# Optimization experiments

Measured on AMD Instinct MI355X. Metric: run time of the kernel, lower is better.

Reference implementation:

```python
import jax, jax.numpy as jnp
import numpy as np

N_NODES = 100000


def gcn_conv(x, src, dst, W, b, n_nodes):
    """PyG GCNConv: add self-loops, symmetric deg^-1/2 normalization,
    linear transform, scatter-add aggregation, bias."""
    loop = jnp.arange(n_nodes, dtype=src.dtype)
    s = jnp.concatenate([src, loop])
    d = jnp.concatenate([dst, loop])
    # degree of destination nodes (includes self-loops)
    deg = jax.ops.segment_sum(jnp.ones(s.shape[0], dtype=x.dtype), d,
                              num_segments=n_nodes)
    dis = jnp.where(deg > 0, jax.lax.rsqrt(deg), 0.0)  # deg^-1/2
    norm = dis[s] * dis[d]                              # [E+N]
    h = x @ W                                           # [N, out]
    msg = h[s] * norm[:, None]                          # gather + scale
    out = jax.ops.segment_sum(msg, d, num_segments=n_nodes)  # scatter-add
    return out + b


def setup_inputs() -> dict:
    key = jax.random.key(0)
    k1, k2, k3, k4 = jax.random.split(key, 4)
    F_in, H, C = 500, 64, 10
    x = jax.random.normal(k1, (N_NODES, F_in), dtype=jnp.float32)
    edge_index = jax.random.randint(k2, (2, 1600000), 0, N_NODES,
                                    dtype=jnp.int32)
    W1 = jax.random.normal(k3, (F_in, H), dtype=jnp.float32) / np.sqrt(F_in)
    b1 = jnp.zeros((H,), dtype=jnp.float32)
    W2 = jax.random.normal(k4, (H, C), dtype=jnp.float32) / np.sqrt(H)
    b2 = jnp.zeros((C,), dtype=jnp.float32)
    return {"x": x, "edge_index": edge_index,
            "W1": W1, "b1": b1, "W2": W2, "b2": b2}


def reference(x, edge_index, W1, b1, W2, b2):
    src, dst = edge_index[0], edge_index[1]
    h = gcn_conv(x, src, dst, W1, b1, N_NODES)
    h = jax.nn.relu(h)
    # dropout is identity at inference (training=False)
    out = gcn_conv(h, src, dst, W2, b2, N_NODES)
    return out
```

## Files before the change

### kernel.cpp

```cpp
#include <hip/hip_runtime.h>

#define F_IN 500
#define HDIM 64
#define CDIM 10
#define KPAD 512
#define NSTAGE 16

typedef __attribute__((ext_vector_type(8))) short bf16x8;
typedef __attribute__((ext_vector_type(4))) float floatx4;

__device__ inline unsigned short f2bf(float f) {
    unsigned int u = __float_as_uint(f);
    u += 0x7fffu + ((u >> 16) & 1u);
    return (unsigned short)(u >> 16);
}

__global__ void deg_count_kernel(const int* __restrict__ dst, int E,
                                 int* __restrict__ deg) {
    int e = blockIdx.x * blockDim.x + threadIdx.x;
    if (e < E) atomicAdd(&deg[dst[e]], 1);
}

__global__ void scan_block_kernel(const int* __restrict__ deg,
                                  int* __restrict__ row_ptr,
                                  int* __restrict__ blk_sum,
                                  float* __restrict__ dis, int Np1) {
    __shared__ int wsum[16];
    int i = blockIdx.x * 1024 + threadIdx.x;
    int v = (i < Np1 - 1) ? deg[i] : 0;
    if (i < Np1 - 1) dis[i] = rsqrtf((float)(v + 1));
    int lane = threadIdx.x & 63;
    int wid = threadIdx.x >> 6;
    int x = v;
#pragma unroll
    for (int off = 1; off < 64; off <<= 1) {
        int y = __shfl_up(x, off);
        if (lane >= off) x += y;
    }
    if (lane == 63) wsum[wid] = x;
    __syncthreads();
    if (threadIdx.x < 16) {
        int ws = wsum[threadIdx.x];
#pragma unroll
        for (int off = 1; off < 16; off <<= 1) {
            int y = __shfl_up(ws, off);
            if ((int)threadIdx.x >= off) ws += y;
        }
        wsum[threadIdx.x] = ws;
    }
    __syncthreads();
    int wp = (wid > 0) ? wsum[wid - 1] : 0;
    if (i < Np1) row_ptr[i] = wp + x - v;
    if (threadIdx.x == 1023) blk_sum[blockIdx.x] = wp + x;
}

__global__ void scan_top_kernel(int* __restrict__ blk_sum, int nb) {
    int carry = 0;
    for (int base = 0; base < nb; base += 64) {
        int i = base + (int)threadIdx.x;
        int v = (i < nb) ? blk_sum[i] : 0;
        int x = v;
#pragma unroll
        for (int off = 1; off < 64; off <<= 1) {
            int y = __shfl_up(x, off);
            if ((int)threadIdx.x >= off) x += y;
        }
        if (i < nb) blk_sum[i] = carry + x - v;
        carry += __shfl(x, 63);
    }
}

__global__ void scan_add_kernel(int* __restrict__ row_ptr,
                                const int* __restrict__ blk_sum, int Np1) {
    int i = blockIdx.x * blockDim.x + threadIdx.x;
    if (i < Np1) row_ptr[i] += blk_sum[i >> 10];
}

__global__ void csr_fill_kernel(const int* __restrict__ src,
                                const int* __restrict__ dst,
                                const int* __restrict__ row_ptr,
                                int* __restrict__ cursor,
                                int* __restrict__ csr_src, int E) {
    int e = blockIdx.x * blockDim.x + threadIdx.x;
    if (e >= E) return;
    int d = dst[e];
    int pos = atomicAdd(&cursor[d], 1);
    csr_src[row_ptr[d] + pos] = src[e];
}

__global__ void wprep_kernel(const float* __restrict__ W1,
                             unsigned short* __restrict__ whf,
                             unsigned short* __restrict__ wlf) {
    int idx = blockIdx.x * 256 + threadIdx.x;
    if (idx >= KPAD * HDIM) return;
    int k = idx >> 6;
    int f = idx & 63;
    float w = (k < F_IN) ? W1[k * HDIM + f] : 0.f;
    unsigned int b = __float_as_uint(w);
    unsigned short hh = (unsigned short)(b >> 16);
    float wl = w - __uint_as_float(b & 0xffff0000u);
    unsigned short ll = (unsigned short)(__float_as_uint(wl) >> 16);
    int kb = k >> 5, q = (k >> 3) & 3, j = k & 7;
    int fb = f >> 4, fl = f & 15;
    int lane = (q << 4) | fl;
    size_t o = ((((size_t)kb * 4 + fb) * 64 + lane) << 3) | (size_t)j;
    whf[o] = hh;
    wlf[o] = ll;
}

__global__ __launch_bounds__(256) void gemm1_kernel(
        const float* __restrict__ x,
        const unsigned short* __restrict__ whf,
        const unsigned short* __restrict__ wlf,
        const float* __restrict__ dis,
        unsigned short* __restrict__ h1b, int N) {
    const int lane = threadIdx.x & 63;
    const int wid = (blockIdx.x * 256 + threadIdx.x) >> 6;
    const int n0 = wid * 32;
    if (n0 >= N) return;
    const int q = lane >> 4;
    const int fl = lane & 15;

    int r0 = n0 + fl;       if (r0 >= N) r0 = N - 1;
    int r1 = n0 + 16 + fl;  if (r1 >= N) r1 = N - 1;
    const float* xp0 = x + (size_t)r0 * F_IN + q * 8;
    const float* xp1 = x + (size_t)r1 * F_IN + q * 8;

    floatx4 acc[2][4];
#pragma unroll
    for (int t = 0; t < 2; ++t)
#pragma unroll
        for (int fb = 0; fb < 4; ++fb) acc[t][fb] = (floatx4){0.f, 0.f, 0.f, 0.f};

    const bf16x8* whv = (const bf16x8*)whf;
    const bf16x8* wlv = (const bf16x8*)wlf;

    for (int kb = 0; kb < NSTAGE; ++kb) {
        float xv0[8], xv1[8];
        if (kb < NSTAGE - 1) {
            float4 a = *(const float4*)(xp0 + kb * 32);
            float4 b = *(const float4*)(xp0 + kb * 32 + 4);
            xv0[0] = a.x; xv0[1] = a.y; xv0[2] = a.z; xv0[3] = a.w;
            xv0[4] = b.x; xv0[5] = b.y; xv0[6] = b.z; xv0[7] = b.w;
            float4 c = *(const float4*)(xp1 + kb * 32);
            float4 d = *(const float4*)(xp1 + kb * 32 + 4);
            xv1[0] = c.x; xv1[1] = c.y; xv1[2] = c.z; xv1[3] = c.w;
            xv1[4] = d.x; xv1[5] = d.y; xv1[6] = d.z; xv1[7] = d.w;
        } else {
#pragma unroll
            for (int j = 0; j < 8; ++j) {
                int kk = kb * 32 + q * 8 + j;
                xv0[j] = (kk < F_IN) ? xp0[kb * 32 + j] : 0.f;
                xv1[j] = (kk < F_IN) ? xp1[kb * 32 + j] : 0.f;
            }
        }
        bf16x8 xh0, xl0, xh1, xl1;
#pragma unroll
        for (int j = 0; j < 8; ++j) {
            unsigned int b0 = __float_as_uint(xv0[j]);
            xh0[j] = (short)(b0 >> 16);
            float res0 = xv0[j] - __uint_as_float(b0 & 0xffff0000u);
            xl0[j] = (short)(__float_as_uint(res0) >> 16);
            unsigned int b1 = __float_as_uint(xv1[j]);
            xh1[j] = (short)(b1 >> 16);
            float res1 = xv1[j] - __uint_as_float(b1 & 0xffff0000u);
            xl1[j] = (short)(__float_as_uint(res1) >> 16);
        }
#pragma unroll
        for (int fb = 0; fb < 4; ++fb) {
            bf16x8 bh = whv[(size_t)(kb * 4 + fb) * 64 + lane];
            bf16x8 bl = wlv[(size_t)(kb * 4 + fb) * 64 + lane];
            acc[0][fb] = __builtin_amdgcn_mfma_f32_16x16x32_bf16(xh0, bh, acc[0][fb], 0, 0, 0);
            acc[0][fb] = __builtin_amdgcn_mfma_f32_16x16x32_bf16(xl0, bh, acc[0][fb], 0, 0, 0);
            acc[0][fb] = __builtin_amdgcn_mfma_f32_16x16x32_bf16(xh0, bl, acc[0][fb], 0, 0, 0);
            acc[1][fb] = __builtin_amdgcn_mfma_f32_16x16x32_bf16(xh1, bh, acc[1][fb], 0, 0, 0);
            acc[1][fb] = __builtin_amdgcn_mfma_f32_16x16x32_bf16(xl1, bh, acc[1][fb], 0, 0, 0);
            acc[1][fb] = __builtin_amdgcn_mfma_f32_16x16x32_bf16(xh1, bl, acc[1][fb], 0, 0, 0);
        }
    }
#pragma unroll
    for (int t = 0; t < 2; ++t) {
#pragma unroll
        for (int r = 0; r < 4; ++r) {
            int node = n0 + t * 16 + q * 4 + r;
            if (node < N) {
                float dn = dis[node];
#pragma unroll
                for (int fb = 0; fb < 4; ++fb) {
                    h1b[(size_t)node * HDIM + fb * 16 + fl] =
                        f2bf(acc[t][fb][r] * dn);
                }
            }
        }
    }
}

__global__ void gather1_kernel(const int* __restrict__ row_ptr,
                               const int* __restrict__ csr_src,
                               const float* __restrict__ dis,
                               const unsigned short* __restrict__ h1b,
                               float* __restrict__ agg1, int N) {
    int nid = blockIdx.x * 4 + (threadIdx.x >> 6);
    if (nid >= N) return;
    int node = __builtin_amdgcn_readfirstlane(nid);
    int lane = threadIdx.x & 63;
    int half = lane >> 5;
    int c = lane & 31;
    int beg = row_ptr[node];
    int end = row_ptr[node + 1];
    float dd = dis[node];
    float a0 = 0.f, a1 = 0.f;
    if (half == 0) {
        unsigned int w = *reinterpret_cast<const unsigned int*>(
            h1b + (size_t)node * HDIM + 2 * c);
        a0 = __uint_as_float(w << 16);
        a1 = __uint_as_float(w & 0xffff0000u);
    }
    int p = beg + half;
    for (; p + 6 < end; p += 8) {
        int s0 = csr_src[p];
        int s1 = csr_src[p + 2];
        int s2 = csr_src[p + 4];
        int s3 = csr_src[p + 6];
        unsigned int w0 = *reinterpret_cast<const unsigned int*>(h1b + (size_t)s0 * HDIM + 2 * c);
        unsigned int w1 = *reinterpret_cast<const unsigned int*>(h1b + (size_t)s1 * HDIM + 2 * c);
        unsigned int w2 = *reinterpret_cast<const unsigned int*>(h1b + (size_t)s2 * HDIM + 2 * c);
        unsigned int w3 = *reinterpret_cast<const unsigned int*>(h1b + (size_t)s3 * HDIM + 2 * c);
        a0 += __uint_as_float(w0 << 16);
        a1 += __uint_as_float(w0 & 0xffff0000u);
        a0 += __uint_as_float(w1 << 16);
        a1 += __uint_as_float(w1 & 0xffff0000u);
        a0 += __uint_as_float(w2 << 16);
        a1 += __uint_as_float(w2 & 0xffff0000u);
        a0 += __uint_as_float(w3 << 16);
        a1 += __uint_as_float(w3 & 0xffff0000u);
    }
    for (; p < end; p += 2) {
        int s0 = csr_src[p];
        unsigned int w0 = *reinterpret_cast<const unsigned int*>(h1b + (size_t)s0 * HDIM + 2 * c);
        a0 += __uint_as_float(w0 << 16);
        a1 += __uint_as_float(w0 & 0xffff0000u);
    }
    a0 += __shfl_xor(a0, 32);
    a1 += __shfl_xor(a1, 32);
    if (half == 0) {
        *reinterpret_cast<float2*>(agg1 + (size_t)node * HDIM + 2 * c) =
            make_float2(a0 * dd, a1 * dd);
    }
}

__global__ void layer2_kernel(const float* __restrict__ agg1,
                              const float* __restrict__ b1,
                              const float* __restrict__ W2,
                              const float* __restrict__ dis,
                              float* __restrict__ h2s, int N) {
    int n = blockIdx.x * blockDim.x + threadIdx.x;
    if (n >= N) return;
    const float* ar = agg1 + (size_t)n * HDIM;
    float t[HDIM];
#pragma unroll
    for (int c = 0; c < HDIM; ++c) {
        float v = ar[c] + b1[c];
        t[c] = v > 0.f ? v : 0.f;
    }
    float dn = dis[n];
    float* h2r = h2s + (size_t)n * CDIM;
#pragma unroll
    for (int j = 0; j < CDIM; ++j) {
        float acc = 0.f;
#pragma unroll
        for (int c = 0; c < HDIM; ++c) acc = fmaf(t[c], W2[c * CDIM + j], acc);
        h2r[j] = acc * dn;
    }
}

__global__ void gather2_kernel(const int* __restrict__ row_ptr,
                               const int* __restrict__ csr_src,
                               const float* __restrict__ dis,
                               const float* __restrict__ h2s,
                               const float* __restrict__ b2,
                               float* __restrict__ out, int N) {
    int nid = blockIdx.x * 4 + (threadIdx.x >> 6);
    if (nid >= N) return;
    int node = __builtin_amdgcn_readfirstlane(nid);
    int lane = threadIdx.x & 63;
    int g = lane >> 4;
    int j = lane & 15;
    int jj = (j < CDIM) ? j : CDIM - 1;
    int beg = row_ptr[node];
    int end = row_ptr[node + 1];
    float acc = 0.f;
    for (int p = beg + g; p < end; p += 4) {
        int s = csr_src[p];
        acc += h2s[(size_t)s * CDIM + jj];
    }
    acc += __shfl_xor(acc, 16);
    acc += __shfl_xor(acc, 32);
    if (lane < CDIM) {
        float dd = dis[node];
        out[(size_t)node * CDIM + lane] =
            b2[lane] + dd * (acc + h2s[(size_t)node * CDIM + lane]);
    }
}

static inline char* align256(char* p) {
    return (char*)(((uintptr_t)p + 255) & ~(uintptr_t)255);
}

extern "C" void kernel_launch(void* const* d_in, const int* in_sizes, int n_in,
                              void* d_out, int out_size, void* d_ws,
                              size_t ws_size, hipStream_t stream) {
    const float* x  = (const float*)d_in[0];
    const int*   ei = (const int*)d_in[1];
    const float* W1 = (const float*)d_in[2];
    const float* b1 = (const float*)d_in[3];
    const float* W2 = (const float*)d_in[4];
    const float* b2 = (const float*)d_in[5];

    const int N = in_sizes[0] / F_IN;
    const int E = in_sizes[1] / 2;
    const int* src = ei;
    const int* dst = ei + E;
    float* out = (float*)d_out;

    const int Np1 = N + 1;
    const int nscan_blocks = (Np1 + 1023) / 1024;

    char* w = (char*)d_ws;
    int* deg = (int*)w;                  w = align256(w + (size_t)N * 4);
    int* cursor = (int*)w;               w = align256(w + (size_t)N * 4);
    float* dis = (float*)w;              w = align256(w + (size_t)N * 4);
    int* row_ptr = (int*)w;              w = align256(w + (size_t)(N + 4) * 4);
    int* blk_sum = (int*)w;              w = align256(w + (size_t)nscan_blocks * 4);
    int* csr_src = (int*)w;              w = align256(w + (size_t)E * 4);
    unsigned short* whf = (unsigned short*)w;  w = align256(w + (size_t)KPAD * HDIM * 2);
    unsigned short* wlf = (unsigned short*)w;  w = align256(w + (size_t)KPAD * HDIM * 2);
    unsigned short* h1b = (unsigned short*)w;  w = align256(w + (size_t)N * HDIM * 2);
    float* agg1 = (float*)w;             w = align256(w + (size_t)N * HDIM * 4);
    float* h2s = (float*)h1b;

    hipMemsetAsync(deg, 0, (size_t)N * 2 * 4, stream);
    hipMemsetAsync(cursor, 0, (size_t)N * 4, stream);

    wprep_kernel<<<(KPAD * HDIM + 255) / 256, 256, 0, stream>>>(W1, whf, wlf);
    deg_count_kernel<<<(E + 255) / 256, 256, 0, stream>>>(dst, E, deg);
    scan_block_kernel<<<nscan_blocks, 1024, 0, stream>>>(deg, row_ptr, blk_sum,
                                                         dis, Np1);
    scan_top_kernel<<<1, 64, 0, stream>>>(blk_sum, nscan_blocks);
    scan_add_kernel<<<(Np1 + 255) / 256, 256, 0, stream>>>(row_ptr, blk_sum,
                                                           Np1);
    csr_fill_kernel<<<(E + 255) / 256, 256, 0, stream>>>(src, dst, row_ptr,
                                                         cursor, csr_src, E);
    {
        int nwaves = (N + 31) / 32;
        int blocks = (nwaves + 3) / 4;
        gemm1_kernel<<<blocks, 256, 0, stream>>>(x, whf, wlf, dis, h1b, N);
    }
    gather1_kernel<<<(N + 3) / 4, 256, 0, stream>>>(row_ptr, csr_src, dis, h1b,
                                                    agg1, N);
    layer2_kernel<<<(N + 255) / 256, 256, 0, stream>>>(agg1, b1, W2, dis, h2s,
                                                       N);
    gather2_kernel<<<(N + 3) / 4, 256, 0, stream>>>(row_ptr, csr_src, dis, h2s,
                                                    b2, out, N);
}
```

Before: 587.4 us.

## Merge prep, CSR fill and GEMM launches; pad h2 rows; deepen gather unrolling

```diff
diff --git a/kernel.cpp b/kernel.cpp
--- a/kernel.cpp
+++ b/kernel.cpp
@@ -5,6 +5,7 @@
 #define CDIM 10
 #define KPAD 512
 #define NSTAGE 16
+#define H2LD 16
 
 typedef __attribute__((ext_vector_type(8))) short bf16x8;
 typedef __attribute__((ext_vector_type(4))) float floatx4;
@@ -14,11 +15,34 @@
     u += 0x7fffu + ((u >> 16) & 1u);
     return (unsigned short)(u >> 16);
 }
-
-__global__ void deg_count_kernel(const int* __restrict__ dst, int E,
-                                 int* __restrict__ deg) {
-    int e = blockIdx.x * blockDim.x + threadIdx.x;
-    if (e < E) atomicAdd(&deg[dst[e]], 1);
+__device__ inline float bflo(unsigned int u) { return __uint_as_float(u << 16); }
+__device__ inline float bfhi(unsigned int u) { return __uint_as_float(u & 0xffff0000u); }
+
+__global__ __launch_bounds__(256) void prep_kernel(
+        const int* __restrict__ dst, int E, int* __restrict__ deg,
+        const float* __restrict__ W1, unsigned short* __restrict__ whf,
+        unsigned short* __restrict__ wlf, int degB) {
+    int bid = blockIdx.x;
+    if (bid < degB) {
+        int e = bid * 256 + threadIdx.x;
+        if (e < E) atomicAdd(&deg[dst[e]], 1);
+    } else {
+        int idx = (bid - degB) * 256 + threadIdx.x;
+        if (idx >= KPAD * HDIM) return;
+        int k = idx >> 6;
+        int f = idx & 63;
+        float w = (k < F_IN) ? W1[k * HDIM + f] : 0.f;
+        unsigned int b = __float_as_uint(w);
+        unsigned short hh = (unsigned short)(b >> 16);
+        float wl = w - __uint_as_float(b & 0xffff0000u);
+        unsigned short ll = (unsigned short)(__float_as_uint(wl) >> 16);
+        int kb = k >> 5, q = (k >> 3) & 3, j = k & 7;
+        int fb = f >> 4, fl = f & 15;
+        int lane = (q << 4) | fl;
+        size_t o = ((((size_t)kb * 4 + fb) * 64 + lane) << 3) | (size_t)j;
+        whf[o] = hh;
+        wlf[o] = ll;
+    }
 }
 
 __global__ void scan_block_kernel(const int* __restrict__ deg,
@@ -70,52 +94,25 @@
     }
 }
 
-__global__ void scan_add_kernel(int* __restrict__ row_ptr,
-                                const int* __restrict__ blk_sum, int Np1) {
-    int i = blockIdx.x * blockDim.x + threadIdx.x;
-    if (i < Np1) row_ptr[i] += blk_sum[i >> 10];
-}
-
-__global__ void csr_fill_kernel(const int* __restrict__ src,
-                                const int* __restrict__ dst,
-                                const int* __restrict__ row_ptr,
-                                int* __restrict__ cursor,
-                                int* __restrict__ csr_src, int E) {
-    int e = blockIdx.x * blockDim.x + threadIdx.x;
-    if (e >= E) return;
-    int d = dst[e];
-    int pos = atomicAdd(&cursor[d], 1);
-    csr_src[row_ptr[d] + pos] = src[e];
-}
-
-__global__ void wprep_kernel(const float* __restrict__ W1,
-                             unsigned short* __restrict__ whf,
-                             unsigned short* __restrict__ wlf) {
-    int idx = blockIdx.x * 256 + threadIdx.x;
-    if (idx >= KPAD * HDIM) return;
-    int k = idx >> 6;
-    int f = idx & 63;
-    float w = (k < F_IN) ? W1[k * HDIM + f] : 0.f;
-    unsigned int b = __float_as_uint(w);
-    unsigned short hh = (unsigned short)(b >> 16);
-    float wl = w - __uint_as_float(b & 0xffff0000u);
-    unsigned short ll = (unsigned short)(__float_as_uint(wl) >> 16);
-    int kb = k >> 5, q = (k >> 3) & 3, j = k & 7;
-    int fb = f >> 4, fl = f & 15;
-    int lane = (q << 4) | fl;
-    size_t o = ((((size_t)kb * 4 + fb) * 64 + lane) << 3) | (size_t)j;
-    whf[o] = hh;
-    wlf[o] = ll;
-}
-
-__global__ __launch_bounds__(256) void gemm1_kernel(
-        const float* __restrict__ x,
-        const unsigned short* __restrict__ whf,
-        const unsigned short* __restrict__ wlf,
-        const float* __restrict__ dis,
-        unsigned short* __restrict__ h1b, int N) {
+__global__ __launch_bounds__(256) void csr_gemm_kernel(
+        const float* __restrict__ x, const unsigned short* __restrict__ whf,
+        const unsigned short* __restrict__ wlf, const float* __restrict__ dis,
+        unsigned short* __restrict__ h1b, int N,
+        const int* __restrict__ src, const int* __restrict__ dst,
+        const int* __restrict__ row_ptr, const int* __restrict__ blk_sum,
+        int* __restrict__ cursor, int* __restrict__ csr_src, int E,
+        int gemmB) {
+    const int bid = blockIdx.x;
+    if (bid >= gemmB) {
+        int e = (bid - gemmB) * 256 + threadIdx.x;
+        if (e >= E) return;
+        int d = dst[e];
+        int pos = atomicAdd(&cursor[d], 1);
+        csr_src[row_ptr[d] + blk_sum[d >> 10] + pos] = src[e];
+        return;
+    }
     const int lane = threadIdx.x & 63;
-    const int wid = (blockIdx.x * 256 + threadIdx.x) >> 6;
+    const int wid = (bid * 256 + threadIdx.x) >> 6;
     const int n0 = wid * 32;
     if (n0 >= N) return;
     const int q = lane >> 4;
@@ -195,51 +192,48 @@
     }
 }
 
-__global__ void gather1_kernel(const int* __restrict__ row_ptr,
-                               const int* __restrict__ csr_src,
-                               const float* __restrict__ dis,
-                               const unsigned short* __restrict__ h1b,
-                               float* __restrict__ agg1, int N) {
+__global__ __launch_bounds__(256) void gather1_kernel(
+        const int* __restrict__ row_ptr, const int* __restrict__ blk_sum,
+        const int* __restrict__ csr_src, const float* __restrict__ dis,
+        const unsigned short* __restrict__ h1b,
+        float* __restrict__ agg1, int N) {
     int nid = blockIdx.x * 4 + (threadIdx.x >> 6);
     if (nid >= N) return;
     int node = __builtin_amdgcn_readfirstlane(nid);
     int lane = threadIdx.x & 63;
     int half = lane >> 5;
     int c = lane & 31;
-    int beg = row_ptr[node];
-    int end = row_ptr[node + 1];
+    int beg = row_ptr[node] + blk_sum[node >> 10];
+    int end = row_ptr[node + 1] + blk_sum[(node + 1) >> 10];
     float dd = dis[node];
     float a0 = 0.f, a1 = 0.f;
     if (half == 0) {
         unsigned int w = *reinterpret_cast<const unsigned int*>(
             h1b + (size_t)node * HDIM + 2 * c);
-        a0 = __uint_as_float(w << 16);
-        a1 = __uint_as_float(w & 0xffff0000u);
+        a0 = bflo(w);
+        a1 = bfhi(w);
     }
     int p = beg + half;
-    for (; p + 6 < end; p += 8) {
-        int s0 = csr_src[p];
-        int s1 = csr_src[p + 2];
-        int s2 = csr_src[p + 4];
-        int s3 = csr_src[p + 6];
-        unsigned int w0 = *reinterpret_cast<const unsigned int*>(h1b + (size_t)s0 * HDIM + 2 * c);
-        unsigned int w1 = *reinterpret_cast<const unsigned int*>(h1b + (size_t)s1 * HDIM + 2 * c);
-        unsigned int w2 = *reinterpret_cast<const unsigned int*>(h1b + (size_t)s2 * HDIM + 2 * c);
-        unsigned int w3 = *reinterpret_cast<const unsigned int*>(h1b + (size_t)s3 * HDIM + 2 * c);
-        a0 += __uint_as_float(w0 << 16);
-        a1 += __uint_as_float(w0 & 0xffff0000u);
-        a0 += __uint_as_float(w1 << 16);
-        a1 += __uint_as_float(w1 & 0xffff0000u);
-        a0 += __uint_as_float(w2 << 16);
-        a1 += __uint_as_float(w2 & 0xffff0000u);
-        a0 += __uint_as_float(w3 << 16);
-        a1 += __uint_as_float(w3 & 0xffff0000u);
+    for (; p + 14 < end; p += 16) {
+        unsigned int wv[8];
+#pragma unroll
+        for (int i = 0; i < 8; ++i) {
+            int s = csr_src[p + 2 * i];
+            wv[i] = *reinterpret_cast<const unsigned int*>(
+                h1b + (size_t)s * HDIM + 2 * c);
+        }
+#pragma unroll
+        for (int i = 0; i < 8; ++i) {
+            a0 += bflo(wv[i]);
+            a1 += bfhi(wv[i]);
+        }
     }
     for (; p < end; p += 2) {
         int s0 = csr_src[p];
-        unsigned int w0 = *reinterpret_cast<const unsigned int*>(h1b + (size_t)s0 * HDIM + 2 * c);
-        a0 += __uint_as_float(w0 << 16);
-        a1 += __uint_as_float(w0 & 0xffff0000u);
+        unsigned int w0 = *reinterpret_cast<const unsigned int*>(
+            h1b + (size_t)s0 * HDIM + 2 * c);
+        a0 += bflo(w0);
+        a1 += bfhi(w0);
     }
     a0 += __shfl_xor(a0, 32);
     a1 += __shfl_xor(a1, 32);
@@ -264,7 +258,7 @@
         t[c] = v > 0.f ? v : 0.f;
     }
     float dn = dis[n];
-    float* h2r = h2s + (size_t)n * CDIM;
+    float* h2r = h2s + (size_t)n * H2LD;
 #pragma unroll
     for (int j = 0; j < CDIM; ++j) {
         float acc = 0.f;
@@ -274,32 +268,42 @@
     }
 }
 
-__global__ void gather2_kernel(const int* __restrict__ row_ptr,
-                               const int* __restrict__ csr_src,
-                               const float* __restrict__ dis,
-                               const float* __restrict__ h2s,
-                               const float* __restrict__ b2,
-                               float* __restrict__ out, int N) {
+__global__ __launch_bounds__(256) void gather2_kernel(
+        const int* __restrict__ row_ptr, const int* __restrict__ blk_sum,
+        const int* __restrict__ csr_src, const float* __restrict__ dis,
+        const float* __restrict__ h2s, const float* __restrict__ b2,
+        float* __restrict__ out, int N) {
     int nid = blockIdx.x * 4 + (threadIdx.x >> 6);
     if (nid >= N) return;
     int node = __builtin_amdgcn_readfirstlane(nid);
     int lane = threadIdx.x & 63;
     int g = lane >> 4;
     int j = lane & 15;
-    int jj = (j < CDIM) ? j : CDIM - 1;
-    int beg = row_ptr[node];
-    int end = row_ptr[node + 1];
+    int beg = row_ptr[node] + blk_sum[node >> 10];
+    int end = row_ptr[node + 1] + blk_sum[(node + 1) >> 10];
     float acc = 0.f;
-    for (int p = beg + g; p < end; p += 4) {
-        int s = csr_src[p];
-        acc += h2s[(size_t)s * CDIM + jj];
+    int p = beg + g;
+    for (; p + 12 < end; p += 16) {
+        int s0 = csr_src[p];
+        int s1 = csr_src[p + 4];
+        int s2 = csr_src[p + 8];
+        int s3 = csr_src[p + 12];
+        float v0 = (j < CDIM) ? h2s[(size_t)s0 * H2LD + j] : 0.f;
+        float v1 = (j < CDIM) ? h2s[(size_t)s1 * H2LD + j] : 0.f;
+        float v2 = (j < CDIM) ? h2s[(size_t)s2 * H2LD + j] : 0.f;
+        float v3 = (j < CDIM) ? h2s[(size_t)s3 * H2LD + j] : 0.f;
+        acc += (v0 + v1) + (v2 + v3);
+    }
+    for (; p < end; p += 4) {
+        int s0 = csr_src[p];
+        acc += (j < CDIM) ? h2s[(size_t)s0 * H2LD + j] : 0.f;
     }
     acc += __shfl_xor(acc, 16);
     acc += __shfl_xor(acc, 32);
     if (lane < CDIM) {
         float dd = dis[node];
         out[(size_t)node * CDIM + lane] =
-            b2[lane] + dd * (acc + h2s[(size_t)node * CDIM + lane]);
+            b2[lane] + dd * (acc + h2s[(size_t)node * H2LD + lane]);
     }
 }
 
@@ -329,6 +333,7 @@
     char* w = (char*)d_ws;
     int* deg = (int*)w;                  w = align256(w + (size_t)N * 4);
     int* cursor = (int*)w;               w = align256(w + (size_t)N * 4);
+    char* zero_end = w;
     float* dis = (float*)w;              w = align256(w + (size_t)N * 4);
     int* row_ptr = (int*)w;              w = align256(w + (size_t)(N + 4) * 4);
     int* blk_sum = (int*)w;              w = align256(w + (size_t)nscan_blocks * 4);
@@ -337,29 +342,28 @@
     unsigned short* wlf = (unsigned short*)w;  w = align256(w + (size_t)KPAD * HDIM * 2);
     unsigned short* h1b = (unsigned short*)w;  w = align256(w + (size_t)N * HDIM * 2);
     float* agg1 = (float*)w;             w = align256(w + (size_t)N * HDIM * 4);
-    float* h2s = (float*)h1b;
-
-    hipMemsetAsync(deg, 0, (size_t)N * 2 * 4, stream);
-    hipMemsetAsync(cursor, 0, (size_t)N * 4, stream);
-
-    wprep_kernel<<<(KPAD * HDIM + 255) / 256, 256, 0, stream>>>(W1, whf, wlf);
-    deg_count_kernel<<<(E + 255) / 256, 256, 0, stream>>>(dst, E, deg);
+    float* h2s = (float*)w;              w = align256(w + (size_t)N * H2LD * 4);
+
+    hipMemsetAsync(deg, 0, (size_t)(zero_end - (char*)deg), stream);
+
+    const int degB = (E + 255) / 256;
+    const int wprepB = (KPAD * HDIM + 255) / 256;
+    prep_kernel<<<degB + wprepB, 256, 0, stream>>>(dst, E, deg, W1, whf, wlf,
+                                                   degB);
     scan_block_kernel<<<nscan_blocks, 1024, 0, stream>>>(deg, row_ptr, blk_sum,
                                                          dis, Np1);
     scan_top_kernel<<<1, 64, 0, stream>>>(blk_sum, nscan_blocks);
-    scan_add_kernel<<<(Np1 + 255) / 256, 256, 0, stream>>>(row_ptr, blk_sum,
-                                                           Np1);
-    csr_fill_kernel<<<(E + 255) / 256, 256, 0, stream>>>(src, dst, row_ptr,
-                                                         cursor, csr_src, E);
     {
-        int nwaves = (N + 31) / 32;
-        int blocks = (nwaves + 3) / 4;
-        gemm1_kernel<<<blocks, 256, 0, stream>>>(x, whf, wlf, dis, h1b, N);
-    }
-    gather1_kernel<<<(N + 3) / 4, 256, 0, stream>>>(row_ptr, csr_src, dis, h1b,
-                                                    agg1, N);
+        int gemmB = ((N + 31) / 32 + 3) / 4;
+        int csrB = (E + 255) / 256;
+        csr_gemm_kernel<<<gemmB + csrB, 256, 0, stream>>>(
+            x, whf, wlf, dis, h1b, N,
+            src, dst, row_ptr, blk_sum, cursor, csr_src, E, gemmB);
+    }
+    gather1_kernel<<<(N + 3) / 4, 256, 0, stream>>>(row_ptr, blk_sum, csr_src,
+                                                    dis, h1b, agg1, N);
     layer2_kernel<<<(N + 255) / 256, 256, 0, stream>>>(agg1, b1, W2, dis, h2s,
                                                        N);
-    gather2_kernel<<<(N + 3) / 4, 256, 0, stream>>>(row_ptr, csr_src, dis, h2s,
-                                                    b2, out, N);
-}
+    gather2_kernel<<<(N + 3) / 4, 256, 0, stream>>>(row_ptr, blk_sum, csr_src,
+                                                    dis, h2s, b2, out, N);
+}
```

Measured after the change: 563.2 us. -4.1%, faster.
